# Optimization experiments

Measured on AMD Instinct MI355X. Metric: run time of the kernel, lower is better.

The kernel has to match this reference:

```python
import jax, jax.numpy as jnp
import numpy as np

N = 64000            # total nodes (64 graphs x 1000 nodes)
E = 1048576          # edges (~16 avg degree)
NB_NODES = 1000
NUM_GRAPHS = 64
F_IN, H1, H2, H3, OUT = 128, 256, 256, 128, 64


def setup_inputs() -> dict:
    key = jax.random.key(0)
    ks = jax.random.split(key, 12)
    x = jax.random.normal(ks[0], (N, F_IN), dtype=jnp.float32)
    # random edges within each graph: pick graph per edge, then local src/dst
    g = jax.random.randint(ks[1], (E,), 0, NUM_GRAPHS)
    src = g * NB_NODES + jax.random.randint(ks[2], (E,), 0, NB_NODES)
    dst = g * NB_NODES + jax.random.randint(ks[3], (E,), 0, NB_NODES)
    edge_index = jnp.stack([src, dst]).astype(jnp.int64)
    batch = (jnp.arange(N) // NB_NODES).astype(jnp.int64)  # sorted graph ids
    def glorot(k, fan_in, fan_out):
        s = jnp.sqrt(6.0 / (fan_in + fan_out))
        return jax.random.uniform(k, (fan_in, fan_out), jnp.float32, -s, s)
    return {
        "x": x, "edge_index": edge_index, "batch": batch,
        "W1": glorot(ks[4], F_IN, H1), "b1": jnp.zeros((H1,), jnp.float32),
        "W2": glorot(ks[5], H1, H2),   "b2": jnp.zeros((H2,), jnp.float32),
        "W3": glorot(ks[6], H2, H3),   "b3": jnp.zeros((H3,), jnp.float32),
        "Wfc": glorot(ks[7], H3 * NB_NODES, OUT),
        "bfc": jnp.zeros((OUT,), jnp.float32),
    }


def _gcn_norm(edge_index, n):
    # add self-loops, symmetric normalization D^-1/2 (A+I) D^-1/2
    loop = jnp.arange(n, dtype=edge_index.dtype)
    src = jnp.concatenate([edge_index[0], loop])
    dst = jnp.concatenate([edge_index[1], loop])
    deg = jax.ops.segment_sum(jnp.ones_like(src, jnp.float32), dst, num_segments=n)
    dinv = 1.0 / jnp.sqrt(deg)  # deg >= 1 thanks to self-loops
    norm = dinv[src] * dinv[dst]
    return src, dst, norm


def _gcn_layer(h, W, b, src, dst, norm, n):
    hl = h @ W                                   # [N, H]
    msg = hl[src] * norm[:, None]                # gather + scale
    agg = jax.ops.segment_sum(msg, dst, num_segments=n)  # scatter-add
    return agg + b


def reference(x, edge_index, batch, W1, b1, W2, b2, W3, b3, Wfc, bfc):
    n = x.shape[0]
    src, dst, norm = _gcn_norm(edge_index, n)
    h = jnp.tanh(_gcn_layer(x, W1, b1, src, dst, norm, n))
    h = jnp.tanh(_gcn_layer(h, W2, b2, src, dst, norm, n))
    h = jnp.tanh(_gcn_layer(h, W3, b3, src, dst, norm, n))
    # batch is sorted with equal graph sizes -> the per-graph loop/concat
    # in the original is exactly a reshape to [num_graphs, nodes*H3]
    h_concat = h.reshape(NUM_GRAPHS, NB_NODES * H3)
    return h_concat @ Wfc + bfc
```

## Files before the change

kernel.cpp:

```cpp
#include <hip/hip_runtime.h>
#include <math.h>

#define N_NODES 64000
#define N_EDGES 1048576
#define NB 1000
#define NG 64
#define NOUT 64
#define FC_SPLIT 500
#define BK_CAP 18000

typedef __attribute__((ext_vector_type(8))) short bfrag;
typedef __attribute__((ext_vector_type(4))) float f32x4;
typedef __attribute__((ext_vector_type(2))) float f32x2;

__device__ inline float bf2f(unsigned short u) {
    union { unsigned int i; float f; } x; x.i = ((unsigned int)u) << 16; return x.f;
}
__device__ inline float bflo(unsigned int u) {
    union { unsigned int i; float f; } x; x.i = u << 16; return x.f;
}
__device__ inline float bfhi(unsigned int u) {
    union { unsigned int i; float f; } x; x.i = u & 0xffff0000u; return x.f;
}
__device__ inline f32x2 upk(unsigned int u) {
    f32x2 r; r.x = bflo(u); r.y = bfhi(u); return r;
}
__device__ inline unsigned short f2bf(float f) {
    union { float f; unsigned int i; } x; x.f = f;
    return (unsigned short)((x.i + 0x7FFFu + ((x.i >> 16) & 1u)) >> 16);
}
__device__ inline int swz(int row, int g) { return g ^ (row & 7) ^ (g >> 3); }


__global__ __launch_bounds__(256) void k_bucket(const int* __restrict__ src,
                                                const int* __restrict__ dst,
                                                int* __restrict__ gcnt,
                                                unsigned int* __restrict__ bucket) {
    __shared__ int lcnt[64];
    __shared__ int lbase[64];
    __shared__ int lcur[64];
    int t = threadIdx.x;
    int e0 = blockIdx.x * 4096;
    if (t < 64) { lcnt[t] = 0; lcur[t] = 0; }
    __syncthreads();
    for (int i = t; i < 4096; i += 256) {
        int d = dst[e0 + i];
        int g = d / NB;
        atomicAdd(&lcnt[g], 1);
    }
    __syncthreads();
    if (t < 64) lbase[t] = atomicAdd(&gcnt[t], lcnt[t]);
    __syncthreads();
    for (int i = t; i < 4096; i += 256) {
        int d = dst[e0 + i];
        int s = src[e0 + i];
        int g = d / NB;
        int pos = atomicAdd(&lcur[g], 1);
        unsigned int packed = ((unsigned int)(d - g * NB) << 10) | (unsigned int)(s - g * NB);
        bucket[(size_t)g * BK_CAP + lbase[g] + pos] = packed;
    }
}

__global__ __launch_bounds__(1024) void k_build(const int* __restrict__ gcnt,
                                                const unsigned int* __restrict__ bucket,
                                                int* __restrict__ rowptr,
                                                int* __restrict__ rowend,
                                                float* __restrict__ dinv,
                                                unsigned short* __restrict__ colp) {
    __shared__ int ind[1024];
    __shared__ int tmp[1024];
    int t = threadIdx.x;
    int g = blockIdx.x;
    int cnt = gcnt[g];
    size_t base = (size_t)g * BK_CAP;
    ind[t] = 0;
    __syncthreads();
    for (int i = t; i < cnt; i += 1024) {
        unsigned int p = bucket[base + i];
        atomicAdd(&ind[p >> 10], 1);
    }
    __syncthreads();
    int deg = ind[t];
    if (t < NB) dinv[g * NB + t] = rsqrtf((float)(deg + 1));
    tmp[t] = deg;
    __syncthreads();
    for (int off = 1; off < 1024; off <<= 1) {
        int o = (t >= off) ? tmp[t - off] : 0;
        __syncthreads();
        tmp[t] += o;
        __syncthreads();
    }
    int excl = tmp[t] - deg;
    if (t < NB) {
        rowptr[g * NB + t] = (int)base + excl;
        rowend[g * NB + t] = (int)base + excl + deg;
    }
    ind[t] = excl;
    __syncthreads();
    for (int i = t; i < cnt; i += 1024) {
        unsigned int p = bucket[base + i];
        int dl = p >> 10;
        int pos = atomicAdd(&ind[dl], 1);
        colp[base + pos] = (unsigned short)(p & 1023u);
    }
}


__global__ void k_cast_scale(const float* __restrict__ in, const float* __restrict__ dinv,
                             unsigned short* __restrict__ out) {
    int i = (blockIdx.x * blockDim.x + threadIdx.x) * 4;
    float d = dinv[i >> 7];
    float4 v = *(const float4*)(in + i);
    union { unsigned short s[4]; uint2 u; } o;
    o.s[0] = f2bf(v.x * d); o.s[1] = f2bf(v.y * d);
    o.s[2] = f2bf(v.z * d); o.s[3] = f2bf(v.w * d);
    *(uint2*)(out + i) = o.u;
}

__global__ void k_wt(const float* __restrict__ W, unsigned short* __restrict__ Wt,
                     int K, int N) {
    int i = blockIdx.x * 256 + threadIdx.x;
    if (i < K * N) {
        int n = i / K, k = i % K;
        Wt[i] = f2bf(W[k * N + n]);
    }
}


template <int H, bool TANH>
__global__ void k_agg(const unsigned short* __restrict__ hs, unsigned short* __restrict__ op,
                      const int* __restrict__ rowptr, const int* __restrict__ rowend,
                      const unsigned short* __restrict__ col,
                      const float* __restrict__ dinv, const float* __restrict__ bias) {
    constexpr int VEC = H / 64;
    int lane = threadIdx.x & 63;
    int b = blockIdx.x;
    int c = b & 7;
    int j = b >> 3;
    int g = c + 8 * (j / 250);
    int chunk = j % 250;
    int v = g * NB + chunk * 4 + (threadIdx.x >> 6);
    const unsigned short* gb = hs + (size_t)g * NB * H;
    f32x2 a0, a1;
    {
        const unsigned short* r = hs + (size_t)v * H + lane * VEC;
        if (VEC == 2) {
            a0 = upk(*(const unsigned int*)r);
        } else {
            uint2 u = *(const uint2*)r;
            a0 = upk(u.x); a1 = upk(u.y);
        }
    }
    int beg = rowptr[v], end = rowend[v];
    for (int e0 = beg; e0 < end; e0 += 64) {
        int me = e0 + lane;
        int s = (me < end) ? (int)col[me] : 0;
        int cnt = min(64, end - e0);
        int i = 0;
        for (; i + 8 <= cnt; i += 8) {
            int sx[8];
#pragma unroll
            for (int q = 0; q < 8; ++q) sx[q] = __builtin_amdgcn_readlane(s, i + q);
            if (VEC == 2) {
                unsigned int u[8];
#pragma unroll
                for (int q = 0; q < 8; ++q)
                    u[q] = *(const unsigned int*)(gb + (size_t)sx[q] * H + lane * 2);
#pragma unroll
                for (int q = 0; q < 8; ++q) a0 += upk(u[q]);
            } else {
                uint2 u[8];
#pragma unroll
                for (int q = 0; q < 8; ++q)
                    u[q] = *(const uint2*)(gb + (size_t)sx[q] * H + lane * 4);
#pragma unroll
                for (int q = 0; q < 8; ++q) { a0 += upk(u[q].x); a1 += upk(u[q].y); }
            }
        }
        for (; i + 4 <= cnt; i += 4) {
            int sx[4];
#pragma unroll
            for (int q = 0; q < 4; ++q) sx[q] = __builtin_amdgcn_readlane(s, i + q);
            if (VEC == 2) {
                unsigned int u[4];
#pragma unroll
                for (int q = 0; q < 4; ++q)
                    u[q] = *(const unsigned int*)(gb + (size_t)sx[q] * H + lane * 2);
#pragma unroll
                for (int q = 0; q < 4; ++q) a0 += upk(u[q]);
            } else {
                uint2 u[4];
#pragma unroll
                for (int q = 0; q < 4; ++q)
                    u[q] = *(const uint2*)(gb + (size_t)sx[q] * H + lane * 4);
#pragma unroll
                for (int q = 0; q < 4; ++q) { a0 += upk(u[q].x); a1 += upk(u[q].y); }
            }
        }
        for (; i < cnt; ++i) {
            int ss = __builtin_amdgcn_readlane(s, i);
            if (VEC == 2) {
                a0 += upk(*(const unsigned int*)(gb + (size_t)ss * H + lane * 2));
            } else {
                uint2 u = *(const uint2*)(gb + (size_t)ss * H + lane * 4);
                a0 += upk(u.x); a1 += upk(u.y);
            }
        }
    }
    float dv = dinv[v];
    float acc[4];
    acc[0] = a0.x; acc[1] = a0.y;
    if (VEC == 4) { acc[2] = a1.x; acc[3] = a1.y; }
    if (TANH) {
#pragma unroll
        for (int q = 0; q < VEC; ++q) acc[q] = tanhf(acc[q] * dv + bias[lane * VEC + q]);
    } else {
#pragma unroll
        for (int q = 0; q < VEC; ++q) acc[q] *= dv;
    }
    unsigned short* o = op + (size_t)v * H + lane * VEC;
    if (VEC == 2) {
        union { unsigned short s[2]; unsigned int u; } pk;
        pk.s[0] = f2bf(acc[0]); pk.s[1] = f2bf(acc[1]);
        *(unsigned int*)o = pk.u;
    } else {
        union { unsigned short s[4]; uint2 u; } pk;
        pk.s[0] = f2bf(acc[0]); pk.s[1] = f2bf(acc[1]);
        pk.s[2] = f2bf(acc[2]); pk.s[3] = f2bf(acc[3]);
        *(uint2*)o = pk.u;
    }
}


__global__ __launch_bounds__(256) void k_gemm1(const unsigned short* __restrict__ A,
                                               const unsigned short* __restrict__ W1t,
                                               const float* __restrict__ b1,
                                               const float* __restrict__ dinv,
                                               unsigned short* __restrict__ C) {
    constexpr int K = 128, N = 256;
    __shared__ unsigned short at[64 * 136];
    int t = threadIdx.x;
    int w = t >> 6, l = t & 63;
    int lm = l & 15, lq = l >> 4;
    int m0 = blockIdx.x * 64;
    int n0 = w * 64;
    {
        int row = t >> 2, kc = (t & 3) * 32;
        const unsigned short* gr = A + (size_t)(m0 + row) * K + kc;
        unsigned short* lr = at + row * 136 + kc;
        uint4 v0 = *(const uint4*)(gr);
        uint4 v1 = *(const uint4*)(gr + 8);
        uint4 v2 = *(const uint4*)(gr + 16);
        uint4 v3 = *(const uint4*)(gr + 24);
        *(uint4*)(lr) = v0; *(uint4*)(lr + 8) = v1;
        *(uint4*)(lr + 16) = v2; *(uint4*)(lr + 24) = v3;
    }
    __syncthreads();
    f32x4 acc[4][4] = {};
    const unsigned short* Bb = W1t + (size_t)(n0 + lm) * K + lq * 8;
    bfrag bfb[2][4];
#pragma unroll
    for (int j = 0; j < 4; ++j) bfb[0][j] = *(const bfrag*)(Bb + (size_t)j * 16 * K);
#pragma unroll
    for (int it = 0; it < K / 32; ++it) {
        int ks = it * 32, cur = it & 1;
        if (it + 1 < K / 32) {
#pragma unroll
            for (int j = 0; j < 4; ++j)
                bfb[cur ^ 1][j] = *(const bfrag*)(Bb + (size_t)j * 16 * K + ks + 32);
        }
        bfrag af[4];
#pragma unroll
        for (int i = 0; i < 4; ++i) af[i] = *(const bfrag*)&at[(i * 16 + lm) * 136 + ks + lq * 8];
#pragma unroll
        for (int i = 0; i < 4; ++i)
#pragma unroll
            for (int j = 0; j < 4; ++j)
                acc[i][j] = __builtin_amdgcn_mfma_f32_16x16x32_bf16(af[i], bfb[cur][j], acc[i][j], 0, 0, 0);
    }
    float bj[4];
#pragma unroll
    for (int j = 0; j < 4; ++j) bj[j] = b1[n0 + j * 16 + lm];
    int row0 = lq * 4;
    float drow[4][4];
#pragma unroll
    for (int i = 0; i < 4; ++i)
#pragma unroll
        for (int r = 0; r < 4; ++r) drow[i][r] = dinv[m0 + i * 16 + row0 + r];
#pragma unroll
    for (int i = 0; i < 4; ++i)
#pragma unroll
        for (int j = 0; j < 4; ++j)
#pragma unroll
            for (int r = 0; r < 4; ++r) {
                float v = tanhf(acc[i][j][r] + bj[j]) * drow[i][r];
                C[(size_t)(m0 + i * 16 + row0 + r) * N + n0 + j * 16 + lm] = f2bf(v);
            }
}


__global__ __launch_bounds__(256) void k_gemm23(const unsigned short* __restrict__ A,
                                                const unsigned short* __restrict__ W2t,
                                                const float* __restrict__ b2,
                                                const unsigned short* __restrict__ W3t,
                                                const float* __restrict__ dinv,
                                                unsigned short* __restrict__ C) {
    constexpr int K = 256, N3 = 128;
    __shared__ unsigned short at[64 * 256];
    int t = threadIdx.x;
    int w = t >> 6, l = t & 63;
    int lm = l & 15, lq = l >> 4;
    int m0 = blockIdx.x * 64;
    int n0 = w * 64;
    int row0 = lq * 4;
    {
        int row = t >> 2, c = t & 3;
        const unsigned short* gr = A + (size_t)(m0 + row) * K + c * 64;
        unsigned short* lr = at + row * 256;
        uint4 v[8];
#pragma unroll
        for (int j = 0; j < 8; ++j) v[j] = *(const uint4*)(gr + j * 8);
#pragma unroll
        for (int j = 0; j < 8; ++j) {
            int gidx = c * 8 + j;
            *(uint4*)(lr + swz(row, gidx) * 8) = v[j];
        }
    }
    __syncthreads();
    f32x4 acc[4][4] = {};
    {
        const unsigned short* Bb = W2t + (size_t)(n0 + lm) * K + lq * 8;
        bfrag bfb[2][4];
#pragma unroll
        for (int j = 0; j < 4; ++j) bfb[0][j] = *(const bfrag*)(Bb + (size_t)j * 16 * K);
#pragma unroll
        for (int it = 0; it < K / 32; ++it) {
            int ks = it * 32, cur = it & 1;
            if (it + 1 < K / 32) {
#pragma unroll
                for (int j = 0; j < 4; ++j)
                    bfb[cur ^ 1][j] = *(const bfrag*)(Bb + (size_t)j * 16 * K + ks + 32);
            }
            bfrag af[4];
            int gidx = it * 4 + lq;
#pragma unroll
            for (int i = 0; i < 4; ++i) {
                int row = i * 16 + lm;
                af[i] = *(const bfrag*)&at[row * 256 + swz(row, gidx) * 8];
            }
#pragma unroll
            for (int i = 0; i < 4; ++i)
#pragma unroll
                for (int j = 0; j < 4; ++j)
                    acc[i][j] = __builtin_amdgcn_mfma_f32_16x16x32_bf16(af[i], bfb[cur][j], acc[i][j], 0, 0, 0);
        }
    }
    __syncthreads();
    {
        float bj[4];
#pragma unroll
        for (int j = 0; j < 4; ++j) bj[j] = b2[n0 + j * 16 + lm];
#pragma unroll
        for (int i = 0; i < 4; ++i)
#pragma unroll
            for (int j = 0; j < 4; ++j) {
                int colb = n0 + j * 16 + lm;
                int gidx = colb >> 3, off = colb & 7;
#pragma unroll
                for (int r = 0; r < 4; ++r) {
                    int row = i * 16 + row0 + r;
                    at[row * 256 + swz(row, gidx) * 8 + off] =
                        f2bf(tanhf(acc[i][j][r] + bj[j]));
                }
            }
    }
    __syncthreads();
    {
        f32x4 acc2[4][2] = {};
        int n3 = w * 32;
        const unsigned short* Bb = W3t + (size_t)(n3 + lm) * K + lq * 8;
        bfrag bfb[2][2];
#pragma unroll
        for (int j = 0; j < 2; ++j) bfb[0][j] = *(const bfrag*)(Bb + (size_t)j * 16 * K);
#pragma unroll
        for (int it = 0; it < K / 32; ++it) {
            int ks = it * 32, cur = it & 1;
            if (it + 1 < K / 32) {
#pragma unroll
                for (int j = 0; j < 2; ++j)
                    bfb[cur ^ 1][j] = *(const bfrag*)(Bb + (size_t)j * 16 * K + ks + 32);
            }
            bfrag af[4];
            int gidx = it * 4 + lq;
#pragma unroll
            for (int i = 0; i < 4; ++i) {
                int row = i * 16 + lm;
                af[i] = *(const bfrag*)&at[row * 256 + swz(row, gidx) * 8];
            }
#pragma unroll
            for (int i = 0; i < 4; ++i)
#pragma unroll
                for (int j = 0; j < 2; ++j)
                    acc2[i][j] = __builtin_amdgcn_mfma_f32_16x16x32_bf16(af[i], bfb[cur][j], acc2[i][j], 0, 0, 0);
        }
        float drow[4][4];
#pragma unroll
        for (int i = 0; i < 4; ++i)
#pragma unroll
            for (int r = 0; r < 4; ++r) drow[i][r] = dinv[m0 + i * 16 + row0 + r];
#pragma unroll
        for (int i = 0; i < 4; ++i)
#pragma unroll
            for (int j = 0; j < 2; ++j)
#pragma unroll
                for (int r = 0; r < 4; ++r)
                    C[(size_t)(m0 + i * 16 + row0 + r) * N3 + n3 + j * 16 + lm] =
                        f2bf(acc2[i][j][r] * drow[i][r]);
    }
}


__global__ void k_fc(const unsigned short* __restrict__ A, const float* __restrict__ B,
                     float* __restrict__ part) {
    __shared__ float As[16][68];
    __shared__ float Bs[16][68];
    const int KROW = NB * 128;
    int t = threadIdx.x;
    int tx = t & 15, ty = t >> 4;
    int k0b = blockIdx.x * 256;
    float acc[4][4] = {};
    for (int k0 = k0b; k0 < k0b + 256; k0 += 16) {
        int arow = t >> 2, ak = (t & 3) << 2;
        uint2 ua = *(const uint2*)(A + (size_t)arow * KROW + k0 + ak);
        As[ak + 0][arow] = bflo(ua.x);
        As[ak + 1][arow] = bfhi(ua.x);
        As[ak + 2][arow] = bflo(ua.y);
        As[ak + 3][arow] = bfhi(ua.y);
        int bk = t >> 4, bn4 = (t & 15) << 2;
        *(float4*)&Bs[bk][bn4] = *(const float4*)(B + (size_t)(k0 + bk) * NOUT + bn4);
        __syncthreads();
#pragma unroll
        for (int kk = 0; kk < 16; ++kk) {
            float4 a = *(const float4*)&As[kk][ty << 2];
            float4 b = *(const float4*)&Bs[kk][tx << 2];
            acc[0][0] += a.x * b.x; acc[0][1] += a.x * b.y; acc[0][2] += a.x * b.z; acc[0][3] += a.x * b.w;
            acc[1][0] += a.y * b.x; acc[1][1] += a.y * b.y; acc[1][2] += a.y * b.z; acc[1][3] += a.y * b.w;
            acc[2][0] += a.z * b.x; acc[2][1] += a.z * b.y; acc[2][2] += a.z * b.z; acc[2][3] += a.z * b.w;
            acc[3][0] += a.w * b.x; acc[3][1] += a.w * b.y; acc[3][2] += a.w * b.z; acc[3][3] += a.w * b.w;
        }
        __syncthreads();
    }
    float* po = part + (size_t)blockIdx.x * (NG * NOUT);
#pragma unroll
    for (int i = 0; i < 4; ++i) {
        float4 r;
        r.x = acc[i][0]; r.y = acc[i][1]; r.z = acc[i][2]; r.w = acc[i][3];
        *(float4*)&po[((ty << 2) + i) * NOUT + (tx << 2)] = r;
    }
}

__global__ void k_fc_reduce(const float* __restrict__ part, const float* __restrict__ bfc,
                            float* __restrict__ out) {
    int i = blockIdx.x * blockDim.x + threadIdx.x;
    float s = bfc[i & 63];
    for (int b = 0; b < FC_SPLIT; ++b) s += part[(size_t)b * (NG * NOUT) + i];
    out[i] = s;
}


static inline size_t align256(size_t x) { return (x + 255) & ~(size_t)255; }

extern "C" void kernel_launch(void* const* d_in, const int* in_sizes, int n_in,
                              void* d_out, int out_size, void* d_ws, size_t ws_size,
                              hipStream_t stream) {
    const float* x   = (const float*)d_in[0];
    const int*   ei  = (const int*)d_in[1];
    const int*   src = ei;
    const int*   dst = ei + N_EDGES;
    const float* W1  = (const float*)d_in[3];
    const float* b1  = (const float*)d_in[4];
    const float* W2  = (const float*)d_in[5];
    const float* b2  = (const float*)d_in[6];
    const float* W3  = (const float*)d_in[7];
    const float* b3  = (const float*)d_in[8];
    const float* Wfc = (const float*)d_in[9];
    const float* bfc = (const float*)d_in[10];
    float* out = (float*)d_out;

    char* w = (char*)d_ws;
    unsigned short* P0 = (unsigned short*)w; w += align256((size_t)N_NODES * 256 * 2);
    unsigned short* P1 = (unsigned short*)w; w += align256((size_t)N_NODES * 256 * 2);
    unsigned short* P2 = (unsigned short*)w; w += align256((size_t)N_NODES * 256 * 2);
    int* rowptr = (int*)w;      w += align256((size_t)N_NODES * 4);
    int* rowend = (int*)w;      w += align256((size_t)N_NODES * 4);
    float* dinv = (float*)w;    w += align256((size_t)N_NODES * 4);
    int* gcnt = (int*)w;        w += align256((size_t)NG * 4);
    unsigned int* bucket = (unsigned int*)w; w += align256((size_t)NG * BK_CAP * 4);
    unsigned short* colp = (unsigned short*)w; w += align256((size_t)NG * BK_CAP * 2);
    float* fcpart = (float*)w;  w += align256((size_t)FC_SPLIT * NG * NOUT * 4);
    unsigned short* W1t = (unsigned short*)w; w += align256((size_t)128 * 256 * 2);
    unsigned short* W2t = (unsigned short*)w; w += align256((size_t)256 * 256 * 2);
    unsigned short* W3t = (unsigned short*)w; w += align256((size_t)256 * 128 * 2);

    hipMemsetAsync(gcnt, 0, (size_t)NG * 4, stream);
    k_bucket<<<N_EDGES / 4096, 256, 0, stream>>>(src, dst, gcnt, bucket);
    k_build<<<NG, 1024, 0, stream>>>(gcnt, bucket, rowptr, rowend, dinv, colp);

    k_cast_scale<<<(N_NODES * 128 / 4) / 256, 256, 0, stream>>>(x, dinv, P0);
    k_wt<<<(128 * 256 + 255) / 256, 256, 0, stream>>>(W1, W1t, 128, 256);
    k_wt<<<(256 * 256 + 255) / 256, 256, 0, stream>>>(W2, W2t, 256, 256);
    k_wt<<<(256 * 128 + 255) / 256, 256, 0, stream>>>(W3, W3t, 256, 128);

    k_agg<128, false><<<N_NODES / 4, 256, 0, stream>>>(P0, P1, rowptr, rowend, colp, dinv, nullptr);
    k_gemm1<<<N_NODES / 64, 256, 0, stream>>>(P1, W1t, b1, dinv, P2);

    k_agg<256, false><<<N_NODES / 4, 256, 0, stream>>>(P2, P0, rowptr, rowend, colp, dinv, nullptr);
    k_gemm23<<<N_NODES / 64, 256, 0, stream>>>(P0, W2t, b2, W3t, dinv, P1);

    k_agg<128, true><<<N_NODES / 4, 256, 0, stream>>>(P1, P0, rowptr, rowend, colp, dinv, b3);

    k_fc<<<FC_SPLIT, 256, 0, stream>>>(P0, Wfc, fcpart);
    k_fc_reduce<<<NG * NOUT / 256, 256, 0, stream>>>(fcpart, bfc, out);
}
```

Baseline: 348.3 us.

## Double-buffer GEMM tiles via direct global-to-LDS loads and use fast tanh

Each GEMM block now handles two 64-row tiles. The second tile is prefetched into a second LDS buffer with global_load_lds while the first is computed, and the W1/W2 fragments are kept in registers across both tiles. tanhf is replaced by an exp/rcp approximation in the GEMM epilogues and the final aggregation. This targets load latency and transcendental cost, at the price of more registers and LDS per block (launch bounds of 2 blocks) and half as many blocks. Correctness depends on the swizzled direct-LDS load layout and the hand-written waitcnt counts matching.

After: 333.1 us. -4.4%, faster.

```diff
diff --git a/kernel.cpp b/kernel.cpp
--- a/kernel.cpp
+++ b/kernel.cpp
@@ -29,7 +29,18 @@
     union { float f; unsigned int i; } x; x.f = f;
     return (unsigned short)((x.i + 0x7FFFu + ((x.i >> 16) & 1u)) >> 16);
 }
-__device__ inline int swz(int row, int g) { return g ^ (row & 7) ^ (g >> 3); }
+__device__ inline float tanh_fast(float x) {
+    float e = __expf(2.0f * x);
+    return fmaf(-2.0f, __builtin_amdgcn_rcpf(e + 1.0f), 1.0f);
+}
+__device__ inline int swz32(int row, int g) { return g ^ (row & 7) ^ (g >> 3); }
+__device__ inline int swz16(int row, int g) { return g ^ (row & 7) ^ (g >> 3); }
+
+__device__ inline void gload_lds16(const unsigned short* g, unsigned short* l) {
+    __builtin_amdgcn_global_load_lds(
+        (const __attribute__((address_space(1))) void*)g,
+        (__attribute__((address_space(3))) void*)l, 16, 0, 0);
+}
 
 
 __global__ __launch_bounds__(256) void k_bucket(const int* __restrict__ src,
@@ -213,7 +224,7 @@
     if (VEC == 4) { acc[2] = a1.x; acc[3] = a1.y; }
     if (TANH) {
 #pragma unroll
-        for (int q = 0; q < VEC; ++q) acc[q] = tanhf(acc[q] * dv + bias[lane * VEC + q]);
+        for (int q = 0; q < VEC; ++q) acc[q] = tanh_fast(acc[q] * dv + bias[lane * VEC + q]);
     } else {
 #pragma unroll
         for (int q = 0; q < VEC; ++q) acc[q] *= dv;
@@ -232,134 +243,166 @@
 }
 
 
-__global__ __launch_bounds__(256) void k_gemm1(const unsigned short* __restrict__ A,
-                                               const unsigned short* __restrict__ W1t,
-                                               const float* __restrict__ b1,
-                                               const float* __restrict__ dinv,
-                                               unsigned short* __restrict__ C) {
+__global__ __launch_bounds__(256, 2) void k_gemm1(const unsigned short* __restrict__ A,
+                                                  const unsigned short* __restrict__ W1t,
+                                                  const float* __restrict__ b1,
+                                                  const float* __restrict__ dinv,
+                                                  unsigned short* __restrict__ C) {
     constexpr int K = 128, N = 256;
-    __shared__ unsigned short at[64 * 136];
+    __shared__ unsigned short at[2][64 * 128];
     int t = threadIdx.x;
     int w = t >> 6, l = t & 63;
     int lm = l & 15, lq = l >> 4;
-    int m0 = blockIdx.x * 64;
     int n0 = w * 64;
+    int row0 = lq * 4;
+    int tile0 = blockIdx.x * 2;
+
     {
-        int row = t >> 2, kc = (t & 3) * 32;
-        const unsigned short* gr = A + (size_t)(m0 + row) * K + kc;
-        unsigned short* lr = at + row * 136 + kc;
-        uint4 v0 = *(const uint4*)(gr);
-        uint4 v1 = *(const uint4*)(gr + 8);
-        uint4 v2 = *(const uint4*)(gr + 16);
-        uint4 v3 = *(const uint4*)(gr + 24);
-        *(uint4*)(lr) = v0; *(uint4*)(lr + 8) = v1;
-        *(uint4*)(lr + 16) = v2; *(uint4*)(lr + 24) = v3;
-    }
-    __syncthreads();
-    f32x4 acc[4][4] = {};
-    const unsigned short* Bb = W1t + (size_t)(n0 + lm) * K + lq * 8;
-    bfrag bfb[2][4];
-#pragma unroll
-    for (int j = 0; j < 4; ++j) bfb[0][j] = *(const bfrag*)(Bb + (size_t)j * 16 * K);
-#pragma unroll
-    for (int it = 0; it < K / 32; ++it) {
-        int ks = it * 32, cur = it & 1;
-        if (it + 1 < K / 32) {
+        const unsigned short* Ab = A + (size_t)tile0 * 64 * K;
+#pragma unroll
+        for (int q = 0; q < 4; ++q) {
+            int rbase = w * 16 + q * 4;
+            int row = rbase + (l >> 4);
+            int g = swz16(row, l & 15);
+            gload_lds16(Ab + (size_t)row * K + g * 8, &at[0][rbase * K]);
+        }
+    }
+    bfrag B1[16];
+    {
+        const unsigned short* Bb = W1t + (size_t)(n0 + lm) * K + lq * 8;
+#pragma unroll
+        for (int j = 0; j < 4; ++j)
+#pragma unroll
+            for (int it = 0; it < 4; ++it)
+                B1[j * 4 + it] = *(const bfrag*)(Bb + (size_t)j * 16 * K + it * 32);
+    }
+    float bj[4];
+#pragma unroll
+    for (int j = 0; j < 4; ++j) bj[j] = b1[n0 + j * 16 + lm];
+
+#pragma unroll
+    for (int tt = 0; tt < 2; ++tt) {
+        int m0 = (tile0 + tt) * 64;
+        if (tt == 0) {
+            const unsigned short* Ab = A + (size_t)(tile0 + 1) * 64 * K;
+#pragma unroll
+            for (int q = 0; q < 4; ++q) {
+                int rbase = w * 16 + q * 4;
+                int row = rbase + (l >> 4);
+                int g = swz16(row, l & 15);
+                gload_lds16(Ab + (size_t)row * K + g * 8, &at[1][rbase * K]);
+            }
+            asm volatile("s_waitcnt vmcnt(4)\n\ts_barrier" ::: "memory");
+        } else {
+            asm volatile("s_waitcnt vmcnt(0)\n\ts_barrier" ::: "memory");
+        }
+        const unsigned short* buf = at[tt];
+        f32x4 acc[4][4] = {};
+#pragma unroll
+        for (int it = 0; it < 4; ++it) {
+            bfrag af[4];
+            int gidx = it * 4 + lq;
+#pragma unroll
+            for (int i = 0; i < 4; ++i) {
+                int row = i * 16 + lm;
+                af[i] = *(const bfrag*)&buf[row * K + swz16(row, gidx) * 8];
+            }
+#pragma unroll
+            for (int i = 0; i < 4; ++i)
+#pragma unroll
+                for (int j = 0; j < 4; ++j)
+                    acc[i][j] = __builtin_amdgcn_mfma_f32_16x16x32_bf16(af[i], B1[j * 4 + it], acc[i][j], 0, 0, 0);
+        }
+        float drow[4][4];
+#pragma unroll
+        for (int i = 0; i < 4; ++i)
+#pragma unroll
+            for (int r = 0; r < 4; ++r) drow[i][r] = dinv[m0 + i * 16 + row0 + r];
+#pragma unroll
+        for (int i = 0; i < 4; ++i)
 #pragma unroll
             for (int j = 0; j < 4; ++j)
-                bfb[cur ^ 1][j] = *(const bfrag*)(Bb + (size_t)j * 16 * K + ks + 32);
-        }
-        bfrag af[4];
-#pragma unroll
-        for (int i = 0; i < 4; ++i) af[i] = *(const bfrag*)&at[(i * 16 + lm) * 136 + ks + lq * 8];
-#pragma unroll
-        for (int i = 0; i < 4; ++i)
-#pragma unroll
-            for (int j = 0; j < 4; ++j)
-                acc[i][j] = __builtin_amdgcn_mfma_f32_16x16x32_bf16(af[i], bfb[cur][j], acc[i][j], 0, 0, 0);
-    }
-    float bj[4];
-#pragma unroll
-    for (int j = 0; j < 4; ++j) bj[j] = b1[n0 + j * 16 + lm];
-    int row0 = lq * 4;
-    float drow[4][4];
-#pragma unroll
-    for (int i = 0; i < 4; ++i)
-#pragma unroll
-        for (int r = 0; r < 4; ++r) drow[i][r] = dinv[m0 + i * 16 + row0 + r];
-#pragma unroll
-    for (int i = 0; i < 4; ++i)
-#pragma unroll
-        for (int j = 0; j < 4; ++j)
-#pragma unroll
-            for (int r = 0; r < 4; ++r) {
-                float v = tanhf(acc[i][j][r] + bj[j]) * drow[i][r];
-                C[(size_t)(m0 + i * 16 + row0 + r) * N + n0 + j * 16 + lm] = f2bf(v);
-            }
-}
-
-
-__global__ __launch_bounds__(256) void k_gemm23(const unsigned short* __restrict__ A,
-                                                const unsigned short* __restrict__ W2t,
-                                                const float* __restrict__ b2,
-                                                const unsigned short* __restrict__ W3t,
-                                                const float* __restrict__ dinv,
-                                                unsigned short* __restrict__ C) {
+#pragma unroll
+                for (int r = 0; r < 4; ++r) {
+                    float v = tanh_fast(acc[i][j][r] + bj[j]) * drow[i][r];
+                    C[(size_t)(m0 + i * 16 + row0 + r) * N + n0 + j * 16 + lm] = f2bf(v);
+                }
+    }
+}
+
+
+__global__ __launch_bounds__(256, 2) void k_gemm23(const unsigned short* __restrict__ A,
+                                                   const unsigned short* __restrict__ W2t,
+                                                   const float* __restrict__ b2,
+                                                   const unsigned short* __restrict__ W3t,
+                                                   const float* __restrict__ dinv,
+                                                   unsigned short* __restrict__ C) {
     constexpr int K = 256, N3 = 128;
-    __shared__ unsigned short at[64 * 256];
+    __shared__ unsigned short at[2][64 * 256];
     int t = threadIdx.x;
     int w = t >> 6, l = t & 63;
     int lm = l & 15, lq = l >> 4;
-    int m0 = blockIdx.x * 64;
     int n0 = w * 64;
     int row0 = lq * 4;
+    int tile0 = blockIdx.x * 2;
+
     {
-        int row = t >> 2, c = t & 3;
-        const unsigned short* gr = A + (size_t)(m0 + row) * K + c * 64;
-        unsigned short* lr = at + row * 256;
-        uint4 v[8];
-#pragma unroll
-        for (int j = 0; j < 8; ++j) v[j] = *(const uint4*)(gr + j * 8);
-#pragma unroll
-        for (int j = 0; j < 8; ++j) {
-            int gidx = c * 8 + j;
-            *(uint4*)(lr + swz(row, gidx) * 8) = v[j];
-        }
-    }
-    __syncthreads();
-    f32x4 acc[4][4] = {};
+        const unsigned short* Ab = A + (size_t)tile0 * 64 * K;
+#pragma unroll
+        for (int q = 0; q < 8; ++q) {
+            int rbase = w * 16 + q * 2;
+            int row = rbase + (l >> 5);
+            int g = swz32(row, l & 31);
+            gload_lds16(Ab + (size_t)row * K + g * 8, &at[0][rbase * K]);
+        }
+    }
+    bfrag B1[32];
     {
         const unsigned short* Bb = W2t + (size_t)(n0 + lm) * K + lq * 8;
-        bfrag bfb[2][4];
-#pragma unroll
-        for (int j = 0; j < 4; ++j) bfb[0][j] = *(const bfrag*)(Bb + (size_t)j * 16 * K);
-#pragma unroll
-        for (int it = 0; it < K / 32; ++it) {
-            int ks = it * 32, cur = it & 1;
-            if (it + 1 < K / 32) {
-#pragma unroll
-                for (int j = 0; j < 4; ++j)
-                    bfb[cur ^ 1][j] = *(const bfrag*)(Bb + (size_t)j * 16 * K + ks + 32);
-            }
+#pragma unroll
+        for (int j = 0; j < 4; ++j)
+#pragma unroll
+            for (int it = 0; it < 8; ++it)
+                B1[j * 8 + it] = *(const bfrag*)(Bb + (size_t)j * 16 * K + it * 32);
+    }
+    float bj[4];
+#pragma unroll
+    for (int j = 0; j < 4; ++j) bj[j] = b2[n0 + j * 16 + lm];
+
+#pragma unroll
+    for (int tt = 0; tt < 2; ++tt) {
+        int m0 = (tile0 + tt) * 64;
+        if (tt == 0) {
+            const unsigned short* Ab = A + (size_t)(tile0 + 1) * 64 * K;
+#pragma unroll
+            for (int q = 0; q < 8; ++q) {
+                int rbase = w * 16 + q * 2;
+                int row = rbase + (l >> 5);
+                int g = swz32(row, l & 31);
+                gload_lds16(Ab + (size_t)row * K + g * 8, &at[1][rbase * K]);
+            }
+            asm volatile("s_waitcnt vmcnt(8)\n\ts_barrier" ::: "memory");
+        } else {
+            asm volatile("s_waitcnt vmcnt(0)\n\ts_barrier" ::: "memory");
+        }
+        unsigned short* buf = at[tt];
+        f32x4 acc[4][4] = {};
+#pragma unroll
+        for (int it = 0; it < 8; ++it) {
             bfrag af[4];
             int gidx = it * 4 + lq;
 #pragma unroll
             for (int i = 0; i < 4; ++i) {
                 int row = i * 16 + lm;
-                af[i] = *(const bfrag*)&at[row * 256 + swz(row, gidx) * 8];
+                af[i] = *(const bfrag*)&buf[row * 256 + swz32(row, gidx) * 8];
             }
 #pragma unroll
             for (int i = 0; i < 4; ++i)
 #pragma unroll
                 for (int j = 0; j < 4; ++j)
-                    acc[i][j] = __builtin_amdgcn_mfma_f32_16x16x32_bf16(af[i], bfb[cur][j], acc[i][j], 0, 0, 0);
-        }
-    }
-    __syncthreads();
-    {
-        float bj[4];
-#pragma unroll
-        for (int j = 0; j < 4; ++j) bj[j] = b2[n0 + j * 16 + lm];
+                    acc[i][j] = __builtin_amdgcn_mfma_f32_16x16x32_bf16(af[i], B1[j * 8 + it], acc[i][j], 0, 0, 0);
+        }
+        asm volatile("s_waitcnt lgkmcnt(0)\n\ts_barrier" ::: "memory");
 #pragma unroll
         for (int i = 0; i < 4; ++i)
 #pragma unroll
@@ -369,53 +412,53 @@
 #pragma unroll
                 for (int r = 0; r < 4; ++r) {
                     int row = i * 16 + row0 + r;
-                    at[row * 256 + swz(row, gidx) * 8 + off] =
-                        f2bf(tanhf(acc[i][j][r] + bj[j]));
+                    buf[row * 256 + swz32(row, gidx) * 8 + off] =
+                        f2bf(tanh_fast(acc[i][j][r] + bj[j]));
                 }
             }
-    }
-    __syncthreads();
-    {
-        f32x4 acc2[4][2] = {};
-        int n3 = w * 32;
-        const unsigned short* Bb = W3t + (size_t)(n3 + lm) * K + lq * 8;
-        bfrag bfb[2][2];
-#pragma unroll
-        for (int j = 0; j < 2; ++j) bfb[0][j] = *(const bfrag*)(Bb + (size_t)j * 16 * K);
-#pragma unroll
-        for (int it = 0; it < K / 32; ++it) {
-            int ks = it * 32, cur = it & 1;
-            if (it + 1 < K / 32) {
+        asm volatile("s_waitcnt lgkmcnt(0)\n\ts_barrier" ::: "memory");
+        {
+            f32x4 acc2[4][2] = {};
+            int n3 = w * 32;
+            const unsigned short* Bb = W3t + (size_t)(n3 + lm) * K + lq * 8;
+            bfrag bfb[2][2];
+#pragma unroll
+            for (int j = 0; j < 2; ++j) bfb[0][j] = *(const bfrag*)(Bb + (size_t)j * 16 * K);
+#pragma unroll
+            for (int it = 0; it < 8; ++it) {
+                int ks = it * 32, pc = it & 1;
+                if (it + 1 < 8) {
+#pragma unroll
+                    for (int j = 0; j < 2; ++j)
+                        bfb[pc ^ 1][j] = *(const bfrag*)(Bb + (size_t)j * 16 * K + ks + 32);
+                }
+                bfrag af[4];
+                int gidx = it * 4 + lq;
+#pragma unroll
+                for (int i = 0; i < 4; ++i) {
+                    int row = i * 16 + lm;
+                    af[i] = *(const bfrag*)&buf[row * 256 + swz32(row, gidx) * 8];
+                }
+#pragma unroll
+                for (int i = 0; i < 4; ++i)
+#pragma unroll
+                    for (int j = 0; j < 2; ++j)
+                        acc2[i][j] = __builtin_amdgcn_mfma_f32_16x16x32_bf16(af[i], bfb[pc][j], acc2[i][j], 0, 0, 0);
+            }
+            float drow[4][4];
+#pragma unroll
+            for (int i = 0; i < 4; ++i)
+#pragma unroll
+                for (int r = 0; r < 4; ++r) drow[i][r] = dinv[m0 + i * 16 + row0 + r];
+#pragma unroll
+            for (int i = 0; i < 4; ++i)
 #pragma unroll
                 for (int j = 0; j < 2; ++j)
-                    bfb[cur ^ 1][j] = *(const bfrag*)(Bb + (size_t)j * 16 * K + ks + 32);
-            }
-            bfrag af[4];
-            int gidx = it * 4 + lq;
-#pragma unroll
-            for (int i = 0; i < 4; ++i) {
-                int row = i * 16 + lm;
-                af[i] = *(const bfrag*)&at[row * 256 + swz(row, gidx) * 8];
-            }
-#pragma unroll
-            for (int i = 0; i < 4; ++i)
-#pragma unroll
-                for (int j = 0; j < 2; ++j)
-                    acc2[i][j] = __builtin_amdgcn_mfma_f32_16x16x32_bf16(af[i], bfb[cur][j], acc2[i][j], 0, 0, 0);
-        }
-        float drow[4][4];
-#pragma unroll
-        for (int i = 0; i < 4; ++i)
-#pragma unroll
-            for (int r = 0; r < 4; ++r) drow[i][r] = dinv[m0 + i * 16 + row0 + r];
-#pragma unroll
-        for (int i = 0; i < 4; ++i)
-#pragma unroll
-            for (int j = 0; j < 2; ++j)
-#pragma unroll
-                for (int r = 0; r < 4; ++r)
-                    C[(size_t)(m0 + i * 16 + row0 + r) * N3 + n3 + j * 16 + lm] =
-                        f2bf(acc2[i][j][r] * drow[i][r]);
+#pragma unroll
+                    for (int r = 0; r < 4; ++r)
+                        C[(size_t)(m0 + i * 16 + row0 + r) * N3 + n3 + j * 16 + lm] =
+                            f2bf(acc2[i][j][r] * drow[i][r]);
+        }
     }
 }
 
@@ -512,10 +555,10 @@
     k_wt<<<(256 * 128 + 255) / 256, 256, 0, stream>>>(W3, W3t, 256, 128);
 
     k_agg<128, false><<<N_NODES / 4, 256, 0, stream>>>(P0, P1, rowptr, rowend, colp, dinv, nullptr);
-    k_gemm1<<<N_NODES / 64, 256, 0, stream>>>(P1, W1t, b1, dinv, P2);
+    k_gemm1<<<N_NODES / 128, 256, 0, stream>>>(P1, W1t, b1, dinv, P2);
 
     k_agg<256, false><<<N_NODES / 4, 256, 0, stream>>>(P2, P0, rowptr, rowend, colp, dinv, nullptr);
-    k_gemm23<<<N_NODES / 64, 256, 0, stream>>>(P0, W2t, b2, W3t, dinv, P1);
+    k_gemm23<<<N_NODES / 128, 256, 0, stream>>>(P0, W2t, b2, W3t, dinv, P1);
 
     k_agg<128, true><<<N_NODES / 4, 256, 0, stream>>>(P1, P0, rowptr, rowend, colp, dinv, b3);
 
```
